# Performance work log

Hardware: AMD Instinct MI355X
Metric: run time of the kernel (lower is better)

Reference implementation:

```python
import jax, jax.numpy as jnp
import numpy as np

N = 50000       # nodes
E = 1600000     # edges (before self-loops)
NFEAT = 256
NHID = 8        # hidden units per head
HEADS = 8
NCLASS = 16
L1 = 0.5        # damping lambda layer 1
L2 = 0.5        # damping lambda layer 2
SLOPE = 0.2     # LeakyReLU negative slope (PyG GATConv default)


def setup_inputs() -> dict:
    ks = jax.random.split(jax.random.key(0), 16)
    g = lambda k, shape, fan: jax.random.normal(k, shape, jnp.float32) * (1.0 / np.sqrt(fan))
    return {
        "x": jax.random.normal(ks[0], (N, NFEAT), jnp.float32),
        "edge_index": jax.random.randint(ks[1], (2, E), 0, N, jnp.int64),
        # conv1: GATConv(nfeat -> nhid, heads=HEADS, concat=True)
        "W1": g(ks[2], (NFEAT, HEADS * NHID), NFEAT),
        "a1_src": g(ks[3], (HEADS, NHID), NHID),
        "a1_dst": g(ks[4], (HEADS, NHID), NHID),
        "b1": jnp.zeros((HEADS * NHID,), jnp.float32),
        # conv2: GATConv(nhid*heads -> nclass, heads=1, concat=False)
        "W2": g(ks[5], (HEADS * NHID, NCLASS), HEADS * NHID),
        "a2_src": g(ks[6], (1, NCLASS), NCLASS),
        "a2_dst": g(ks[7], (1, NCLASS), NCLASS),
        "b2": jnp.zeros((NCLASS,), jnp.float32),
        # side-branch linear layers
        "fc1_W": g(ks[8], (NFEAT, NHID), NFEAT),
        "fc1_b": jnp.zeros((NHID,), jnp.float32),
        "fc2_W": g(ks[9], (HEADS * NHID, NCLASS), HEADS * NHID),
        "fc2_b": jnp.zeros((NCLASS,), jnp.float32),
    }


def gat_conv(x, W, a_src, a_dst, b, src, dst, heads, outc, concat):
    n = x.shape[0]
    h = (x @ W).reshape(n, heads, outc)                 # [N, H, C]
    alpha_s = jnp.sum(h * a_src, axis=-1)               # [N, H]
    alpha_d = jnp.sum(h * a_dst, axis=-1)               # [N, H]
    e = jax.nn.leaky_relu(alpha_s[src] + alpha_d[dst], SLOPE)  # [Etot, H]
    # segment softmax over incoming edges of each destination node
    m = jax.ops.segment_max(e, dst, num_segments=n)
    m = jax.lax.stop_gradient(m)                        # max-shift is grad-neutral
    ex = jnp.exp(e - m[dst])
    denom = jax.ops.segment_sum(ex, dst, num_segments=n)
    alpha = ex / denom[dst]                             # [Etot, H]
    out = jax.ops.segment_sum(h[src] * alpha[:, :, None], dst, num_segments=n)
    if concat:
        out = out.reshape(n, heads * outc)
    else:
        out = out.mean(axis=1)
    return out + b


def reference(x, edge_index, W1, a1_src, a1_dst, b1, W2, a2_src, a2_dst, b2,
              fc1_W, fc1_b, fc2_W, fc2_b):
    loop = jnp.arange(N, dtype=edge_index.dtype)
    src = jnp.concatenate([edge_index[0], loop])
    dst = jnp.concatenate([edge_index[1], loop])
    # layer 1: GATConv + damped linear side branch
    out1 = gat_conv(x, W1, a1_src, a1_dst, b1, src, dst, HEADS, NHID, True)
    side1 = jnp.tile(x @ fc1_W + fc1_b, (1, HEADS))     # cat of heads copies
    h = jax.nn.elu(out1 - L1 * side1)                   # [N, H*C]
    # layer 2
    out2 = gat_conv(h, W2, a2_src, a2_dst, b2, src, dst, 1, NCLASS, False)
    side2 = h @ fc2_W + fc2_b
    return jax.nn.log_softmax(out2 - L2 * side2, axis=1)
```

## Files before the change

kernel.cpp:

```cpp
#include <hip/hip_runtime.h>
#include <hip/hip_bf16.h>
#include <cstddef>

constexpr int N      = 50000;
constexpr int E      = 1600000;
constexpr int NFEAT  = 256;
constexpr float SLOPE = 0.2f;
constexpr float L1d  = 0.5f;
constexpr float L2d  = 0.5f;

constexpr int BSHIFT = 7;
constexpr int NBUK   = (N + 127) >> BSHIFT;
constexpr int EPB    = 4096;
constexpr int NBLK   = (E + EPB - 1) / EPB;
constexpr int CAP    = 5120;

constexpr size_t al64(size_t x) { return (x + 63) & ~size_t(63); }
constexpr size_t W_OFFS  = 0;
constexpr size_t W_CSR   = W_OFFS  + al64(N + 1);
constexpr size_t W_STAGE = W_CSR   + (size_t)E;
constexpr size_t W_BHIST = W_STAGE + (size_t)E;
constexpr size_t W_TOT   = W_BHIST + al64((size_t)NBLK * NBUK);
constexpr size_t W_BBASE = W_TOT   + al64(NBUK);
constexpr size_t W_H1B   = W_BBASE + al64(NBUK + 1);
constexpr size_t W_S1B   = W_H1B   + (size_t)N * 32;
constexpr size_t W_D1    = W_S1B   + (size_t)N * 4;
constexpr size_t W_SIDE1 = W_D1    + (size_t)N * 8;
constexpr size_t W_HF    = W_SIDE1 + (size_t)N * 8;
constexpr size_t W_H2B   = W_HF    + (size_t)N * 64;
constexpr size_t W_SIDE2 = W_H2B   + (size_t)N * 8;
constexpr size_t W_S2B   = W_SIDE2 + (size_t)N * 16;
constexpr size_t W_D2    = W_S2B   + al64(N / 2);

typedef short bf16x8 __attribute__((ext_vector_type(8)));
typedef float f32x4  __attribute__((ext_vector_type(4)));

__device__ inline short f2bf(float f) {
    unsigned u = __builtin_bit_cast(unsigned, f);
    u += 0x7FFF + ((u >> 16) & 1);
    return (short)(u >> 16);
}

__device__ inline float bfu2f(unsigned short u) {
    return __builtin_bit_cast(float, (unsigned)u << 16);
}


__global__ __launch_bounds__(256) void p1_hist_kernel(const int* __restrict__ ei,
                                                      int* __restrict__ bhist) {
    __shared__ int hist[NBUK];
    int tid = threadIdx.x;
    for (int j = tid; j < NBUK; j += 256) hist[j] = 0;
    __syncthreads();
    int base = blockIdx.x * EPB;
    int end = base + EPB; if (end > E) end = E;
    for (int i = base + tid; i < end; i += 256) {
        int d = ei[E + i];
        atomicAdd(&hist[d >> BSHIFT], 1);
    }
    __syncthreads();
    for (int j = tid; j < NBUK; j += 256) bhist[(size_t)blockIdx.x * NBUK + j] = hist[j];
}

__global__ __launch_bounds__(512) void s1_scan_kernel(int* __restrict__ bhist,
                                                      int* __restrict__ tot) {
    __shared__ int sd[512];
    int tid = threadIdx.x;
    int b = blockIdx.x;
    int v = (tid < NBLK) ? bhist[(size_t)tid * NBUK + b] : 0;
    sd[tid] = v;
    __syncthreads();
    for (int off = 1; off < 512; off <<= 1) {
        int t = (tid >= off) ? sd[tid - off] : 0;
        __syncthreads();
        sd[tid] += t;
        __syncthreads();
    }
    if (tid < NBLK) bhist[(size_t)tid * NBUK + b] = sd[tid] - v;
    if (tid == 511) tot[b] = sd[511];
}

__global__ __launch_bounds__(512) void s2_scan_kernel(const int* __restrict__ tot,
                                                      int* __restrict__ bbase,
                                                      int* __restrict__ offs) {
    __shared__ int sd[512];
    int tid = threadIdx.x;
    int v = (tid < NBUK) ? tot[tid] : 0;
    sd[tid] = v;
    __syncthreads();
    for (int off = 1; off < 512; off <<= 1) {
        int t = (tid >= off) ? sd[tid - off] : 0;
        __syncthreads();
        sd[tid] += t;
        __syncthreads();
    }
    if (tid < NBUK) bbase[tid] = sd[tid] - v;
    if (tid == 0) { bbase[NBUK] = E; offs[N] = E; }
}

__global__ __launch_bounds__(256) void p2_stage_kernel(const int* __restrict__ ei,
                                                       const int* __restrict__ bhist,
                                                       const int* __restrict__ bbase,
                                                       unsigned int* __restrict__ stage) {
    __shared__ int cur[NBUK];
    int tid = threadIdx.x;
    for (int j = tid; j < NBUK; j += 256)
        cur[j] = bbase[j] + bhist[(size_t)blockIdx.x * NBUK + j];
    __syncthreads();
    int base = blockIdx.x * EPB;
    int end = base + EPB; if (end > E) end = E;
    for (int i = base + tid; i < end; i += 256) {
        int s = ei[i];
        int d = ei[E + i];
        int b = d >> BSHIFT;
        int pos = atomicAdd(&cur[b], 1);
        stage[pos] = ((unsigned int)(d & 127) << 24) | (unsigned int)s;
    }
}

__global__ __launch_bounds__(256) void p3_fine_kernel(const unsigned int* __restrict__ stage,
                                                      const int* __restrict__ bbase,
                                                      int* __restrict__ offs,
                                                      int* __restrict__ csr) {
    __shared__ unsigned int sstage[CAP];
    __shared__ int hist[128];
    __shared__ int scn[128];
    __shared__ int cur[128];
    int tid = threadIdx.x;
    int b = blockIdx.x;
    int ebase = bbase[b], eend = bbase[b + 1];
    int cnt = eend - ebase;
    if (tid < 128) hist[tid] = 0;
    __syncthreads();
    for (int i = tid; i < cnt; i += 256) {
        unsigned int p = stage[ebase + i];
        if (i < CAP) sstage[i] = p;
        atomicAdd(&hist[p >> 24], 1);
    }
    __syncthreads();
    if (tid < 128) scn[tid] = hist[tid];
    __syncthreads();
    for (int off = 1; off < 128; off <<= 1) {
        int t = (tid < 128 && tid >= off) ? scn[tid - off] : 0;
        __syncthreads();
        if (tid < 128) scn[tid] += t;
        __syncthreads();
    }
    if (tid < 128) {
        int excl = scn[tid] - hist[tid];
        cur[tid] = excl;
        int v = (b << BSHIFT) + tid;
        if (v < N) offs[v] = ebase + excl;
    }
    __syncthreads();
    for (int i = tid; i < cnt; i += 256) {
        unsigned int p = (i < CAP) ? sstage[i] : stage[ebase + i];
        int dloc = (int)(p >> 24);
        int s = (int)(p & 0xFFFFFFu);
        int r = atomicAdd(&cur[dloc], 1);
        csr[ebase + r] = s;
    }
}

__global__ __launch_bounds__(256) void gemm1_kernel(const float* __restrict__ x,
                                                    const float* __restrict__ W1,
                                                    const float* __restrict__ fc1W,
                                                    const float* __restrict__ fc1b,
                                                    short* __restrict__ h1b,
                                                    float* __restrict__ side1) {
    __shared__ bf16x8 wfrag[2560];
    int tid = threadIdx.x;

    for (int s = tid; s < 2560; s += 256) {
        int l = s & 63;
        int t = s >> 6;
        int nt = t % 5, kt = t / 5;
        int col = nt * 16 + (l & 15);
        int kbase = kt * 32 + (l >> 4) * 8;
        bf16x8 v;
#pragma unroll
        for (int j = 0; j < 8; ++j) {
            float f = 0.f;
            if (col < 64)      f = W1[(size_t)(kbase + j) * 64 + col];
            else if (col < 72) f = fc1W[(size_t)(kbase + j) * 8 + (col - 64)];
            v[j] = f2bf(f);
        }
        wfrag[s] = v;
    }
    __syncthreads();

    int w = tid >> 6;
    int l = tid & 63;
    int row0 = blockIdx.x * 64;
    int arow = row0 + w * 16 + (l & 15);
    if (arow >= N) arow = N - 1;
    const float* ap = x + (size_t)arow * NFEAT + ((l >> 4) * 8);

    f32x4 acc[5];
#pragma unroll
    for (int nt = 0; nt < 5; ++nt) acc[nt] = (f32x4){0.f, 0.f, 0.f, 0.f};

#pragma unroll
    for (int kt = 0; kt < 8; ++kt) {
        float4 alo = *reinterpret_cast<const float4*>(ap + kt * 32);
        float4 ahi = *reinterpret_cast<const float4*>(ap + kt * 32 + 4);
        bf16x8 af;
        af[0] = f2bf(alo.x); af[1] = f2bf(alo.y); af[2] = f2bf(alo.z); af[3] = f2bf(alo.w);
        af[4] = f2bf(ahi.x); af[5] = f2bf(ahi.y); af[6] = f2bf(ahi.z); af[7] = f2bf(ahi.w);
#pragma unroll
        for (int nt = 0; nt < 5; ++nt) {
            acc[nt] = __builtin_amdgcn_mfma_f32_16x16x32_bf16(
                af, wfrag[(kt * 5 + nt) * 64 + l], acc[nt], 0, 0, 0);
        }
    }

    int cbase = l & 15;
    int rbase = row0 + w * 16 + (l >> 4) * 4;
#pragma unroll
    for (int nt = 0; nt < 4; ++nt) {
#pragma unroll
        for (int r = 0; r < 4; ++r) {
            int row = rbase + r;
            if (row < N) h1b[(size_t)row * 64 + nt * 16 + cbase] = f2bf(acc[nt][r]);
        }
    }
    if (cbase < 8) {
        float bb = fc1b[cbase];
#pragma unroll
        for (int r = 0; r < 4; ++r) {
            int row = rbase + r;
            if (row < N) side1[(size_t)row * 8 + cbase] = acc[4][r] + bb;
        }
    }
}

__global__ __launch_bounds__(256) void alpha1_kernel(const __hip_bfloat16* __restrict__ h1b,
                                                     const float* __restrict__ a1s,
                                                     const float* __restrict__ a1d,
                                                     __hip_bfloat16* __restrict__ s1b,
                                                     float* __restrict__ d1) {
    int wave = threadIdx.x >> 6;
    int lane = threadIdx.x & 63;
    int v = blockIdx.x * 4 + wave;
    if (v >= N) return;
    float hv = __bfloat162float(h1b[(size_t)v * 64 + lane]);
    float sa = hv * a1s[lane];
    float sd = hv * a1d[lane];
#pragma unroll
    for (int off = 1; off < 8; off <<= 1) {
        sa += __shfl_xor(sa, off, 64);
        sd += __shfl_xor(sd, off, 64);
    }
    if ((lane & 7) == 0) {
        s1b[v * 8 + (lane >> 3)] = __float2bfloat16(sa);
        d1[v * 8 + (lane >> 3)] = sd;
    }
}

__global__ __launch_bounds__(256) void agg1_kernel(const int* __restrict__ offs,
                                                   const int* __restrict__ csr,
                                                   const unsigned short* __restrict__ h1u,
                                                   const unsigned short* __restrict__ s1u,
                                                   const float* __restrict__ d1,
                                                   const float* __restrict__ side1,
                                                   const float* __restrict__ b1,
                                                   float* __restrict__ hf) {
    int wave = threadIdx.x >> 6;
    int lane = threadIdx.x & 63;
    int v = blockIdx.x * 4 + wave;
    if (v >= N) return;
    int j  = lane >> 3;
    int hh = lane & 7;
    int hc = lane >> 3;

    float dv_att = d1[v * 8 + hh];
    float dv_ch  = __shfl(dv_att, hc, 64);

    float e0 = bfu2f(s1u[v * 8 + hc]) + dv_ch;
    e0 = fmaxf(e0, SLOPE * e0);
    float ex0 = __expf(e0);
    float acc = ex0 * bfu2f(h1u[(size_t)v * 64 + lane]);
    float den0 = ex0;
    float den_att = 0.f;

    int beg = offs[v], end = offs[v + 1];
    int deg = end - beg;
    int ng = (deg + 7) >> 3;

    auto csrg = [&](int g) {
        int idx = beg + g * 8 + j;
        idx = idx < end - 1 ? idx : end - 1;
        idx = idx > 0 ? idx : 0;
        return csr[idx];
    };

    unsigned short hA[8], hB[8];
    int sA = 0, sB = 0;
    float svA = 0.f, svB = 0.f;

    if (ng > 0) {
        sA = csrg(0);
        svA = bfu2f(s1u[sA * 8 + hh]);
#pragma unroll
        for (int jj = 0; jj < 8; ++jj) {
            int sj = __builtin_amdgcn_readlane(sA, jj * 8);
            const unsigned short* p = h1u + ((size_t)sj << 6);
            hA[jj] = p[lane];
        }
        sB = csrg(1);
    }

    int g = 0;
    for (; g + 1 < ng; g += 2) {
        svB = bfu2f(s1u[sB * 8 + hh]);
#pragma unroll
        for (int jj = 0; jj < 8; ++jj) {
            int sj = __builtin_amdgcn_readlane(sB, jj * 8);
            const unsigned short* p = h1u + ((size_t)sj << 6);
            hB[jj] = p[lane];
        }
        int sC = csrg(g + 2);
        {
            float a = svA + dv_att;
            a = fmaxf(a, SLOPE * a);
            float xv = __expf(a);
            xv = (beg + g * 8 + j < end) ? xv : 0.f;
            den_att += xv;
#pragma unroll
            for (int jj = 0; jj < 8; ++jj) {
                float xj = __shfl(xv, jj * 8 + hc, 64);
                acc += xj * bfu2f(hA[jj]);
            }
        }
        sA = sC;
        svA = bfu2f(s1u[sA * 8 + hh]);
#pragma unroll
        for (int jj = 0; jj < 8; ++jj) {
            int sj = __builtin_amdgcn_readlane(sA, jj * 8);
            const unsigned short* p = h1u + ((size_t)sj << 6);
            hA[jj] = p[lane];
        }
        int sD = csrg(g + 3);
        {
            float a = svB + dv_att;
            a = fmaxf(a, SLOPE * a);
            float xv = __expf(a);
            xv = (beg + (g + 1) * 8 + j < end) ? xv : 0.f;
            den_att += xv;
#pragma unroll
            for (int jj = 0; jj < 8; ++jj) {
                float xj = __shfl(xv, jj * 8 + hc, 64);
                acc += xj * bfu2f(hB[jj]);
            }
        }
        sB = sD;
    }
    if (g < ng) {
        float a = svA + dv_att;
        a = fmaxf(a, SLOPE * a);
        float xv = __expf(a);
        xv = (beg + g * 8 + j < end) ? xv : 0.f;
        den_att += xv;
#pragma unroll
        for (int jj = 0; jj < 8; ++jj) {
            float xj = __shfl(xv, jj * 8 + hc, 64);
            acc += xj * bfu2f(hA[jj]);
        }
    }

    den_att += __shfl_xor(den_att, 8, 64);
    den_att += __shfl_xor(den_att, 16, 64);
    den_att += __shfl_xor(den_att, 32, 64);
    float den = den0 + __shfl(den_att, hc, 64);

    float o = acc / den + b1[lane];
    float z = o - L1d * side1[v * 8 + (lane & 7)];
    hf[(size_t)v * 64 + lane] = z > 0.f ? z : (__expf(z) - 1.f);
}

__global__ __launch_bounds__(256) void gemm2_kernel(const float* __restrict__ hf,
                                                    const float* __restrict__ W2,
                                                    const float* __restrict__ fc2W,
                                                    const float* __restrict__ fc2b,
                                                    __hip_bfloat16* __restrict__ h2b,
                                                    float* __restrict__ side2) {
    __shared__ float xs[128][65];
    __shared__ float ws[64][33];
    int tid = threadIdx.x;
    int ty = tid >> 3;
    int tx = tid & 7;
    int row0 = blockIdx.x * 128;

    float acc[4][4];
#pragma unroll
    for (int i = 0; i < 4; ++i)
#pragma unroll
        for (int j = 0; j < 4; ++j) acc[i][j] = 0.f;

    int lr = tid >> 4;
    int lj = tid & 15;
#pragma unroll
    for (int it = 0; it < 8; ++it) {
        int r = lr + it * 16;
        int grow = row0 + r;
        if (grow >= N) grow = N - 1;
        float4 vv = *reinterpret_cast<const float4*>(&hf[(size_t)grow * 64 + lj * 4]);
        xs[r][lj * 4 + 0] = vv.x;
        xs[r][lj * 4 + 1] = vv.y;
        xs[r][lj * 4 + 2] = vv.z;
        xs[r][lj * 4 + 3] = vv.w;
    }
    for (int idx = tid; idx < 64 * 32; idx += 256) {
        int k = idx >> 5;
        int c = idx & 31;
        float v = (c < 16) ? W2[(size_t)k * 16 + c] : fc2W[(size_t)k * 16 + (c - 16)];
        ws[k][c] = v;
    }
    __syncthreads();
#pragma unroll 4
    for (int k = 0; k < 64; ++k) {
        float xv[4], wv[4];
#pragma unroll
        for (int i = 0; i < 4; ++i) xv[i] = xs[ty * 4 + i][k];
#pragma unroll
        for (int j = 0; j < 4; ++j) wv[j] = ws[k][tx * 4 + j];
#pragma unroll
        for (int i = 0; i < 4; ++i)
#pragma unroll
            for (int j = 0; j < 4; ++j) acc[i][j] += xv[i] * wv[j];
    }

#pragma unroll
    for (int i = 0; i < 4; ++i) {
        int row = row0 + ty * 4 + i;
        if (row >= N) continue;
#pragma unroll
        for (int j = 0; j < 4; ++j) {
            int c = tx * 4 + j;
            if (c < 16) h2b[(size_t)row * 16 + c] = __float2bfloat16(acc[i][j]);
            else        side2[(size_t)row * 16 + (c - 16)] = acc[i][j] + fc2b[c - 16];
        }
    }
}

__global__ __launch_bounds__(256) void alpha2_kernel(const __hip_bfloat16* __restrict__ h2b,
                                                     const float* __restrict__ a2s,
                                                     const float* __restrict__ a2d,
                                                     __hip_bfloat16* __restrict__ s2b,
                                                     float* __restrict__ d2) {
    int wave = threadIdx.x >> 6;
    int lane = threadIdx.x & 63;
    int vbase = (blockIdx.x * 4 + wave) * 4;
    int r = lane >> 4;
    int c = lane & 15;
    int v = vbase + r;
    float hv = (v < N) ? __bfloat162float(h2b[(size_t)v * 16 + c]) : 0.f;
    float sa = hv * a2s[c];
    float sd = hv * a2d[c];
#pragma unroll
    for (int off = 1; off < 16; off <<= 1) {
        sa += __shfl_xor(sa, off, 64);
        sd += __shfl_xor(sd, off, 64);
    }
    if (v < N && c == 0) {
        s2b[v] = __float2bfloat16(sa);
        d2[v] = sd;
    }
}

__global__ __launch_bounds__(256) void agg2_kernel(const int* __restrict__ offs,
                                                   const int* __restrict__ csr,
                                                   const unsigned short* __restrict__ h2u,
                                                   const unsigned short* __restrict__ s2u,
                                                   const float* __restrict__ d2,
                                                   const float* __restrict__ side2,
                                                   const float* __restrict__ b2,
                                                   float* __restrict__ out) {
    int wave = threadIdx.x >> 6;
    int lane = threadIdx.x & 63;
    int v = blockIdx.x * 4 + wave;
    if (v >= N) return;
    int c = lane & 15;
    int slot = lane >> 4;
    float dv = d2[v];

    float acc = 0.f, den = 0.f;
    if (slot == 0) {
        float e = bfu2f(s2u[v]) + dv;
        e = fmaxf(e, SLOPE * e);
        float ex = __expf(e);
        acc = ex * bfu2f(h2u[(size_t)v * 16 + c]);
        den = ex;
    }
    int beg = offs[v], end = offs[v + 1];
    int deg = end - beg;
    int ng = (deg + 3) >> 2;

    auto csrg = [&](int g) {
        int idx = beg + g * 4 + slot;
        idx = idx < end - 1 ? idx : end - 1;
        idx = idx > 0 ? idx : 0;
        return csr[idx];
    };

    int sA = 0, sB = 0;
    float svA = 0.f, svB = 0.f, hvA = 0.f, hvB = 0.f;
    if (ng > 0) {
        sA = csrg(0);
        svA = bfu2f(s2u[sA]);
        hvA = bfu2f(h2u[(size_t)sA * 16 + c]);
        sB = csrg(1);
    }
    int g = 0;
    for (; g + 1 < ng; g += 2) {
        svB = bfu2f(s2u[sB]);
        hvB = bfu2f(h2u[(size_t)sB * 16 + c]);
        int sC = csrg(g + 2);
        {
            float a = svA + dv;
            a = fmaxf(a, SLOPE * a);
            float x = __expf(a);
            x = (beg + g * 4 + slot < end) ? x : 0.f;
            acc += x * hvA;
            den += x;
        }
        sA = sC;
        svA = bfu2f(s2u[sA]);
        hvA = bfu2f(h2u[(size_t)sA * 16 + c]);
        int sD = csrg(g + 3);
        {
            float a = svB + dv;
            a = fmaxf(a, SLOPE * a);
            float x = __expf(a);
            x = (beg + (g + 1) * 4 + slot < end) ? x : 0.f;
            acc += x * hvB;
            den += x;
        }
        sB = sD;
    }
    if (g < ng) {
        float a = svA + dv;
        a = fmaxf(a, SLOPE * a);
        float x = __expf(a);
        x = (beg + g * 4 + slot < end) ? x : 0.f;
        acc += x * hvA;
        den += x;
    }

    acc += __shfl_xor(acc, 16, 64);
    acc += __shfl_xor(acc, 32, 64);
    den += __shfl_xor(den, 16, 64);
    den += __shfl_xor(den, 32, 64);

    float o = acc / den + b2[c];
    float z = o - L2d * side2[(size_t)v * 16 + c];

    float m = z;
#pragma unroll
    for (int off = 1; off < 16; off <<= 1) m = fmaxf(m, __shfl_xor(m, off, 64));
    float ex = __expf(z - m);
    float s = ex;
#pragma unroll
    for (int off = 1; off < 16; off <<= 1) s += __shfl_xor(s, off, 64);
    float lsm = z - m - __logf(s);
    if (slot == 0) out[(size_t)v * 16 + c] = lsm;
}

extern "C" void kernel_launch(void* const* d_in, const int* in_sizes, int n_in,
                              void* d_out, int out_size, void* d_ws, size_t ws_size,
                              hipStream_t stream) {
    const float* x    = (const float*)d_in[0];
    const int*   ei   = (const int*)d_in[1];
    const float* W1   = (const float*)d_in[2];
    const float* a1s  = (const float*)d_in[3];
    const float* a1d  = (const float*)d_in[4];
    const float* b1   = (const float*)d_in[5];
    const float* W2   = (const float*)d_in[6];
    const float* a2s  = (const float*)d_in[7];
    const float* a2d  = (const float*)d_in[8];
    const float* b2   = (const float*)d_in[9];
    const float* fc1W = (const float*)d_in[10];
    const float* fc1b = (const float*)d_in[11];
    const float* fc2W = (const float*)d_in[12];
    const float* fc2b = (const float*)d_in[13];
    float* out = (float*)d_out;

    int*   wsi = (int*)d_ws;
    float* wsf = (float*)d_ws;
    int*   offs   = wsi + W_OFFS;
    int*   csr    = wsi + W_CSR;
    unsigned int* stage = (unsigned int*)(wsi + W_STAGE);
    int*   bhist  = wsi + W_BHIST;
    int*   tot    = wsi + W_TOT;
    int*   bbase  = wsi + W_BBASE;
    __hip_bfloat16* h1b = (__hip_bfloat16*)(wsf + W_H1B);
    __hip_bfloat16* s1b = (__hip_bfloat16*)(wsf + W_S1B);
    float* d1     = wsf + W_D1;
    float* side1  = wsf + W_SIDE1;
    float* hf     = wsf + W_HF;
    __hip_bfloat16* h2b = (__hip_bfloat16*)(wsf + W_H2B);
    float* side2  = wsf + W_SIDE2;
    __hip_bfloat16* s2b = (__hip_bfloat16*)(wsf + W_S2B);
    float* d2     = wsf + W_D2;

    p1_hist_kernel<<<NBLK, 256, 0, stream>>>(ei, bhist);
    s1_scan_kernel<<<NBUK, 512, 0, stream>>>(bhist, tot);
    s2_scan_kernel<<<1, 512, 0, stream>>>(tot, bbase, offs);
    p2_stage_kernel<<<NBLK, 256, 0, stream>>>(ei, bhist, bbase, stage);
    p3_fine_kernel<<<NBUK, 256, 0, stream>>>(stage, bbase, offs, csr);

    gemm1_kernel<<<(N + 63) / 64, 256, 0, stream>>>(x, W1, fc1W, fc1b,
                                                    (short*)h1b, side1);
    alpha1_kernel<<<(N + 3) / 4, 256, 0, stream>>>(h1b, a1s, a1d, s1b, d1);
    agg1_kernel<<<(N + 3) / 4, 256, 0, stream>>>(offs, csr,
                                                 (const unsigned short*)h1b,
                                                 (const unsigned short*)s1b,
                                                 d1, side1, b1, hf);

    gemm2_kernel<<<(N + 127) / 128, 256, 0, stream>>>(hf, W2, fc2W, fc2b, h2b, side2);
    alpha2_kernel<<<(N + 15) / 16, 256, 0, stream>>>(h2b, a2s, a2d, s2b, d2);
    agg2_kernel<<<(N + 3) / 4, 256, 0, stream>>>(offs, csr,
                                                 (const unsigned short*)h2b,
                                                 (const unsigned short*)s2b,
                                                 d2, side2, b2, out);
}
```

Measured before the change: 156.7 us.

## Restructure layer-1 aggregation to per-lane redundant attention with scalar CSR reads

Rewrites the layer-1 aggregation so every lane computes the attention weight for its own head, rather than one lane per edge/head pair followed by shuffle broadcasts. Neighbor indices come from uniform CSR loads via readfirstlane, in groups of four, with a two-stage software pipeline and a scalar tail loop. This removes the per-edge shuffles and the final cross-lane denominator reduction. In exchange it runs eight times as many exp evaluations and issues a separate s1 gather per lane.

```diff
diff --git a/kernel.cpp b/kernel.cpp
--- a/kernel.cpp
+++ b/kernel.cpp
@@ -265,117 +265,92 @@
                                                    const float* __restrict__ side1,
                                                    const float* __restrict__ b1,
                                                    float* __restrict__ hf) {
-    int wave = threadIdx.x >> 6;
     int lane = threadIdx.x & 63;
-    int v = blockIdx.x * 4 + wave;
+    int v = blockIdx.x * 4 + (threadIdx.x >> 6);
     if (v >= N) return;
-    int j  = lane >> 3;
-    int hh = lane & 7;
-    int hc = lane >> 3;
-
-    float dv_att = d1[v * 8 + hh];
-    float dv_ch  = __shfl(dv_att, hc, 64);
-
-    float e0 = bfu2f(s1u[v * 8 + hc]) + dv_ch;
+    int hh = lane >> 3;
+
+    float dv = d1[v * 8 + hh];
+    float e0 = bfu2f(s1u[v * 8 + hh]) + dv;
     e0 = fmaxf(e0, SLOPE * e0);
     float ex0 = __expf(e0);
-    float acc = ex0 * bfu2f(h1u[(size_t)v * 64 + lane]);
-    float den0 = ex0;
-    float den_att = 0.f;
+    float acc = ex0 * bfu2f(h1u[((size_t)v << 6) + lane]);
+    float den = ex0;
 
     int beg = offs[v], end = offs[v + 1];
     int deg = end - beg;
-    int ng = (deg + 7) >> 3;
-
-    auto csrg = [&](int g) {
-        int idx = beg + g * 8 + j;
-        idx = idx < end - 1 ? idx : end - 1;
-        idx = idx > 0 ? idx : 0;
-        return csr[idx];
-    };
-
-    unsigned short hA[8], hB[8];
-    int sA = 0, sB = 0;
-    float svA = 0.f, svB = 0.f;
-
-    if (ng > 0) {
-        sA = csrg(0);
-        svA = bfu2f(s1u[sA * 8 + hh]);
-#pragma unroll
-        for (int jj = 0; jj < 8; ++jj) {
-            int sj = __builtin_amdgcn_readlane(sA, jj * 8);
-            const unsigned short* p = h1u + ((size_t)sj << 6);
-            hA[jj] = p[lane];
-        }
-        sB = csrg(1);
-    }
-
+    int ngf = deg >> 2;
+    const int* cb = csr + beg;
+
+    int sA0, sA1, sA2, sA3, sB0, sB1, sB2, sB3;
+    unsigned short svA0, svA1, svA2, svA3, hvA0, hvA1, hvA2, hvA3;
+    unsigned short svB0, svB1, svB2, svB3, hvB0, hvB1, hvB2, hvB3;
+
+#define RFL4(s0, s1_, s2_, s3_, p)                                           \
+    do {                                                                     \
+        s0  = __builtin_amdgcn_readfirstlane((p)[0]);                        \
+        s1_ = __builtin_amdgcn_readfirstlane((p)[1]);                        \
+        s2_ = __builtin_amdgcn_readfirstlane((p)[2]);                        \
+        s3_ = __builtin_amdgcn_readfirstlane((p)[3]);                        \
+    } while (0)
+
+#define LOADS4(sv0, sv1, sv2, sv3, hv0, hv1, hv2, hv3, s0, s1_, s2_, s3_)    \
+    do {                                                                     \
+        sv0 = s1u[(size_t)(s0) * 8 + hh];                                    \
+        sv1 = s1u[(size_t)(s1_) * 8 + hh];                                   \
+        sv2 = s1u[(size_t)(s2_) * 8 + hh];                                   \
+        sv3 = s1u[(size_t)(s3_) * 8 + hh];                                   \
+        hv0 = h1u[((size_t)(s0) << 6) + lane];                               \
+        hv1 = h1u[((size_t)(s1_) << 6) + lane];                              \
+        hv2 = h1u[((size_t)(s2_) << 6) + lane];                              \
+        hv3 = h1u[((size_t)(s3_) << 6) + lane];                              \
+    } while (0)
+
+#define COMP4(sv0, sv1, sv2, sv3, hv0, hv1, hv2, hv3)                        \
+    do {                                                                     \
+        float a0 = bfu2f(sv0) + dv; a0 = fmaxf(a0, SLOPE * a0);              \
+        float a1 = bfu2f(sv1) + dv; a1 = fmaxf(a1, SLOPE * a1);              \
+        float a2 = bfu2f(sv2) + dv; a2 = fmaxf(a2, SLOPE * a2);              \
+        float a3 = bfu2f(sv3) + dv; a3 = fmaxf(a3, SLOPE * a3);              \
+        float x0 = __expf(a0), x1 = __expf(a1), x2 = __expf(a2), x3 = __expf(a3); \
+        acc += x0 * bfu2f(hv0); den += x0;                                   \
+        acc += x1 * bfu2f(hv1); den += x1;                                   \
+        acc += x2 * bfu2f(hv2); den += x2;                                   \
+        acc += x3 * bfu2f(hv3); den += x3;                                   \
+    } while (0)
+
+    if (ngf > 0) {
+        RFL4(sA0, sA1, sA2, sA3, cb);
+        LOADS4(svA0, svA1, svA2, svA3, hvA0, hvA1, hvA2, hvA3, sA0, sA1, sA2, sA3);
+        if (ngf > 1) RFL4(sB0, sB1, sB2, sB3, cb + 4);
+    }
     int g = 0;
-    for (; g + 1 < ng; g += 2) {
-        svB = bfu2f(s1u[sB * 8 + hh]);
-#pragma unroll
-        for (int jj = 0; jj < 8; ++jj) {
-            int sj = __builtin_amdgcn_readlane(sB, jj * 8);
-            const unsigned short* p = h1u + ((size_t)sj << 6);
-            hB[jj] = p[lane];
-        }
-        int sC = csrg(g + 2);
-        {
-            float a = svA + dv_att;
-            a = fmaxf(a, SLOPE * a);
-            float xv = __expf(a);
-            xv = (beg + g * 8 + j < end) ? xv : 0.f;
-            den_att += xv;
-#pragma unroll
-            for (int jj = 0; jj < 8; ++jj) {
-                float xj = __shfl(xv, jj * 8 + hc, 64);
-                acc += xj * bfu2f(hA[jj]);
-            }
-        }
-        sA = sC;
-        svA = bfu2f(s1u[sA * 8 + hh]);
-#pragma unroll
-        for (int jj = 0; jj < 8; ++jj) {
-            int sj = __builtin_amdgcn_readlane(sA, jj * 8);
-            const unsigned short* p = h1u + ((size_t)sj << 6);
-            hA[jj] = p[lane];
-        }
-        int sD = csrg(g + 3);
-        {
-            float a = svB + dv_att;
-            a = fmaxf(a, SLOPE * a);
-            float xv = __expf(a);
-            xv = (beg + (g + 1) * 8 + j < end) ? xv : 0.f;
-            den_att += xv;
-#pragma unroll
-            for (int jj = 0; jj < 8; ++jj) {
-                float xj = __shfl(xv, jj * 8 + hc, 64);
-                acc += xj * bfu2f(hB[jj]);
-            }
-        }
-        sB = sD;
-    }
-    if (g < ng) {
-        float a = svA + dv_att;
+    for (; g + 1 < ngf; g += 2) {
+        LOADS4(svB0, svB1, svB2, svB3, hvB0, hvB1, hvB2, hvB3, sB0, sB1, sB2, sB3);
+        if (g + 2 < ngf) RFL4(sA0, sA1, sA2, sA3, cb + (g + 2) * 4);
+        COMP4(svA0, svA1, svA2, svA3, hvA0, hvA1, hvA2, hvA3);
+        if (g + 2 < ngf)
+            LOADS4(svA0, svA1, svA2, svA3, hvA0, hvA1, hvA2, hvA3, sA0, sA1, sA2, sA3);
+        if (g + 3 < ngf) RFL4(sB0, sB1, sB2, sB3, cb + (g + 3) * 4);
+        COMP4(svB0, svB1, svB2, svB3, hvB0, hvB1, hvB2, hvB3);
+    }
+    if (g < ngf) COMP4(svA0, svA1, svA2, svA3, hvA0, hvA1, hvA2, hvA3);
+
+    for (int t = ngf * 4; t < deg; ++t) {
+        int s = __builtin_amdgcn_readfirstlane(cb[t]);
+        float a = bfu2f(s1u[(size_t)s * 8 + hh]) + dv;
         a = fmaxf(a, SLOPE * a);
-        float xv = __expf(a);
-        xv = (beg + g * 8 + j < end) ? xv : 0.f;
-        den_att += xv;
-#pragma unroll
-        for (int jj = 0; jj < 8; ++jj) {
-            float xj = __shfl(xv, jj * 8 + hc, 64);
-            acc += xj * bfu2f(hA[jj]);
-        }
-    }
-
-    den_att += __shfl_xor(den_att, 8, 64);
-    den_att += __shfl_xor(den_att, 16, 64);
-    den_att += __shfl_xor(den_att, 32, 64);
-    float den = den0 + __shfl(den_att, hc, 64);
+        float xx = __expf(a);
+        acc += xx * bfu2f(h1u[((size_t)s << 6) + lane]);
+        den += xx;
+    }
+#undef RFL4
+#undef LOADS4
+#undef COMP4
 
     float o = acc / den + b1[lane];
     float z = o - L1d * side1[v * 8 + (lane & 7)];
-    hf[(size_t)v * 64 + lane] = z > 0.f ? z : (__expf(z) - 1.f);
+    hf[((size_t)v << 6) + lane] = z > 0.f ? z : (__expf(z) - 1.f);
 }
 
 __global__ __launch_bounds__(256) void gemm2_kernel(const float* __restrict__ hf,
```

After: 177.7 us. 1.13x slower.

## Store layer-1 output in bf16 and compute layer-2 GEMM with MFMA

Applied to the files above, without the earlier changes.

agg1 now writes the ELU output as bf16 instead of fp32, which halves the intermediate traffic. gemm2 is rewritten to use bf16 MFMA 16x16x32 with the weight fragments preloaded into LDS, replacing the fp32 LDS-tiled scalar GEMM. agg2's edge loop is split into full groups with no per-edge mask or clamping plus one masked remainder pass. The load and compute sequences in agg1 are moved into macros. The cost is extra bf16 rounding of the hidden activations and of W2.

```diff
diff --git a/kernel.cpp b/kernel.cpp
--- a/kernel.cpp
+++ b/kernel.cpp
@@ -26,8 +26,8 @@
 constexpr size_t W_S1B   = W_H1B   + (size_t)N * 32;
 constexpr size_t W_D1    = W_S1B   + (size_t)N * 4;
 constexpr size_t W_SIDE1 = W_D1    + (size_t)N * 8;
-constexpr size_t W_HF    = W_SIDE1 + (size_t)N * 8;
-constexpr size_t W_H2B   = W_HF    + (size_t)N * 64;
+constexpr size_t W_HFB   = W_SIDE1 + (size_t)N * 8;
+constexpr size_t W_H2B   = W_HFB   + (size_t)N * 32;
 constexpr size_t W_SIDE2 = W_H2B   + (size_t)N * 8;
 constexpr size_t W_S2B   = W_SIDE2 + (size_t)N * 16;
 constexpr size_t W_D2    = W_S2B   + al64(N / 2);
@@ -264,7 +264,7 @@
                                                    const float* __restrict__ d1,
                                                    const float* __restrict__ side1,
                                                    const float* __restrict__ b1,
-                                                   float* __restrict__ hf) {
+                                                   short* __restrict__ hfb) {
     int wave = threadIdx.x >> 6;
     int lane = threadIdx.x & 63;
     int v = blockIdx.x * 4 + wave;
@@ -298,75 +298,63 @@
     int sA = 0, sB = 0;
     float svA = 0.f, svB = 0.f;
 
+#define LOADH(s8, h)                                                        \
+    do {                                                                     \
+        int sj0 = __builtin_amdgcn_readlane(s8, 0);                          \
+        int sj1 = __builtin_amdgcn_readlane(s8, 8);                          \
+        int sj2 = __builtin_amdgcn_readlane(s8, 16);                         \
+        int sj3 = __builtin_amdgcn_readlane(s8, 24);                         \
+        int sj4 = __builtin_amdgcn_readlane(s8, 32);                         \
+        int sj5 = __builtin_amdgcn_readlane(s8, 40);                         \
+        int sj6 = __builtin_amdgcn_readlane(s8, 48);                         \
+        int sj7 = __builtin_amdgcn_readlane(s8, 56);                         \
+        h[0] = h1u[((size_t)sj0 << 6) + lane];                               \
+        h[1] = h1u[((size_t)sj1 << 6) + lane];                               \
+        h[2] = h1u[((size_t)sj2 << 6) + lane];                               \
+        h[3] = h1u[((size_t)sj3 << 6) + lane];                               \
+        h[4] = h1u[((size_t)sj4 << 6) + lane];                               \
+        h[5] = h1u[((size_t)sj5 << 6) + lane];                               \
+        h[6] = h1u[((size_t)sj6 << 6) + lane];                               \
+        h[7] = h1u[((size_t)sj7 << 6) + lane];                               \
+    } while (0)
+
+#define COMP(sv, h, gidx)                                                    \
+    do {                                                                     \
+        float a = (sv) + dv_att;                                             \
+        a = fmaxf(a, SLOPE * a);                                             \
+        float xv = __expf(a);                                                \
+        xv = (beg + (gidx) * 8 + j < end) ? xv : 0.f;                        \
+        den_att += xv;                                                       \
+        _Pragma("unroll")                                                    \
+        for (int jj = 0; jj < 8; ++jj) {                                     \
+            float xj = __shfl(xv, jj * 8 + hc, 64);                          \
+            acc += xj * bfu2f(h[jj]);                                        \
+        }                                                                    \
+    } while (0)
+
     if (ng > 0) {
         sA = csrg(0);
         svA = bfu2f(s1u[sA * 8 + hh]);
-#pragma unroll
-        for (int jj = 0; jj < 8; ++jj) {
-            int sj = __builtin_amdgcn_readlane(sA, jj * 8);
-            const unsigned short* p = h1u + ((size_t)sj << 6);
-            hA[jj] = p[lane];
-        }
+        LOADH(sA, hA);
         sB = csrg(1);
     }
 
     int g = 0;
     for (; g + 1 < ng; g += 2) {
         svB = bfu2f(s1u[sB * 8 + hh]);
-#pragma unroll
-        for (int jj = 0; jj < 8; ++jj) {
-            int sj = __builtin_amdgcn_readlane(sB, jj * 8);
-            const unsigned short* p = h1u + ((size_t)sj << 6);
-            hB[jj] = p[lane];
-        }
+        LOADH(sB, hB);
         int sC = csrg(g + 2);
-        {
-            float a = svA + dv_att;
-            a = fmaxf(a, SLOPE * a);
-            float xv = __expf(a);
-            xv = (beg + g * 8 + j < end) ? xv : 0.f;
-            den_att += xv;
-#pragma unroll
-            for (int jj = 0; jj < 8; ++jj) {
-                float xj = __shfl(xv, jj * 8 + hc, 64);
-                acc += xj * bfu2f(hA[jj]);
-            }
-        }
+        COMP(svA, hA, g);
         sA = sC;
         svA = bfu2f(s1u[sA * 8 + hh]);
-#pragma unroll
-        for (int jj = 0; jj < 8; ++jj) {
-            int sj = __builtin_amdgcn_readlane(sA, jj * 8);
-            const unsigned short* p = h1u + ((size_t)sj << 6);
-            hA[jj] = p[lane];
-        }
+        LOADH(sA, hA);
         int sD = csrg(g + 3);
-        {
-            float a = svB + dv_att;
-            a = fmaxf(a, SLOPE * a);
-            float xv = __expf(a);
-            xv = (beg + (g + 1) * 8 + j < end) ? xv : 0.f;
-            den_att += xv;
-#pragma unroll
-            for (int jj = 0; jj < 8; ++jj) {
-                float xj = __shfl(xv, jj * 8 + hc, 64);
-                acc += xj * bfu2f(hB[jj]);
-            }
-        }
+        COMP(svB, hB, g + 1);
         sB = sD;
     }
-    if (g < ng) {
-        float a = svA + dv_att;
-        a = fmaxf(a, SLOPE * a);
-        float xv = __expf(a);
-        xv = (beg + g * 8 + j < end) ? xv : 0.f;
-        den_att += xv;
-#pragma unroll
-        for (int jj = 0; jj < 8; ++jj) {
-            float xj = __shfl(xv, jj * 8 + hc, 64);
-            acc += xj * bfu2f(hA[jj]);
-        }
-    }
+    if (g < ng) COMP(svA, hA, g);
+#undef LOADH
+#undef COMP
 
     den_att += __shfl_xor(den_att, 8, 64);
     den_att += __shfl_xor(den_att, 16, 64);
@@ -375,70 +363,66 @@
 
     float o = acc / den + b1[lane];
     float z = o - L1d * side1[v * 8 + (lane & 7)];
-    hf[(size_t)v * 64 + lane] = z > 0.f ? z : (__expf(z) - 1.f);
-}
-
-__global__ __launch_bounds__(256) void gemm2_kernel(const float* __restrict__ hf,
+    hfb[(size_t)v * 64 + lane] = f2bf(z > 0.f ? z : (__expf(z) - 1.f));
+}
+
+__global__ __launch_bounds__(256) void gemm2_kernel(const unsigned short* __restrict__ hfb,
                                                     const float* __restrict__ W2,
                                                     const float* __restrict__ fc2W,
                                                     const float* __restrict__ fc2b,
-                                                    __hip_bfloat16* __restrict__ h2b,
+                                                    short* __restrict__ h2b,
                                                     float* __restrict__ side2) {
-    __shared__ float xs[128][65];
-    __shared__ float ws[64][33];
+    __shared__ bf16x8 wfrag[256];
     int tid = threadIdx.x;
-    int ty = tid >> 3;
-    int tx = tid & 7;
-    int row0 = blockIdx.x * 128;
-
-    float acc[4][4];
-#pragma unroll
-    for (int i = 0; i < 4; ++i)
-#pragma unroll
-        for (int j = 0; j < 4; ++j) acc[i][j] = 0.f;
-
-    int lr = tid >> 4;
-    int lj = tid & 15;
-#pragma unroll
-    for (int it = 0; it < 8; ++it) {
-        int r = lr + it * 16;
-        int grow = row0 + r;
-        if (grow >= N) grow = N - 1;
-        float4 vv = *reinterpret_cast<const float4*>(&hf[(size_t)grow * 64 + lj * 4]);
-        xs[r][lj * 4 + 0] = vv.x;
-        xs[r][lj * 4 + 1] = vv.y;
-        xs[r][lj * 4 + 2] = vv.z;
-        xs[r][lj * 4 + 3] = vv.w;
-    }
-    for (int idx = tid; idx < 64 * 32; idx += 256) {
-        int k = idx >> 5;
-        int c = idx & 31;
-        float v = (c < 16) ? W2[(size_t)k * 16 + c] : fc2W[(size_t)k * 16 + (c - 16)];
-        ws[k][c] = v;
-    }
-    __syncthreads();
-#pragma unroll 4
-    for (int k = 0; k < 64; ++k) {
-        float xv[4], wv[4];
-#pragma unroll
-        for (int i = 0; i < 4; ++i) xv[i] = xs[ty * 4 + i][k];
-#pragma unroll
-        for (int j = 0; j < 4; ++j) wv[j] = ws[k][tx * 4 + j];
-#pragma unroll
-        for (int i = 0; i < 4; ++i)
-#pragma unroll
-            for (int j = 0; j < 4; ++j) acc[i][j] += xv[i] * wv[j];
-    }
-
-#pragma unroll
-    for (int i = 0; i < 4; ++i) {
-        int row = row0 + ty * 4 + i;
-        if (row >= N) continue;
-#pragma unroll
-        for (int j = 0; j < 4; ++j) {
-            int c = tx * 4 + j;
-            if (c < 16) h2b[(size_t)row * 16 + c] = __float2bfloat16(acc[i][j]);
-            else        side2[(size_t)row * 16 + (c - 16)] = acc[i][j] + fc2b[c - 16];
+
+    if (tid < 256) {
+        int s = tid;
+        int l = s & 63;
+        int t = s >> 6;
+        int nt = t & 1, kt = t >> 1;
+        int col = nt * 16 + (l & 15);
+        int kbase = kt * 32 + (l >> 4) * 8;
+        bf16x8 v;
+#pragma unroll
+        for (int j = 0; j < 8; ++j) {
+            float f = (col < 16) ? W2[(size_t)(kbase + j) * 16 + col]
+                                 : fc2W[(size_t)(kbase + j) * 16 + (col - 16)];
+            v[j] = f2bf(f);
+        }
+        wfrag[s] = v;
+    }
+    __syncthreads();
+
+    int w = tid >> 6;
+    int l = tid & 63;
+    int row0 = blockIdx.x * 64;
+    int arow = row0 + w * 16 + (l & 15);
+    if (arow >= N) arow = N - 1;
+    const unsigned short* ap = hfb + (size_t)arow * 64 + ((l >> 4) * 8);
+
+    f32x4 acc[2];
+    acc[0] = (f32x4){0.f, 0.f, 0.f, 0.f};
+    acc[1] = (f32x4){0.f, 0.f, 0.f, 0.f};
+
+#pragma unroll
+    for (int kt = 0; kt < 2; ++kt) {
+        bf16x8 af = *reinterpret_cast<const bf16x8*>(ap + kt * 32);
+#pragma unroll
+        for (int nt = 0; nt < 2; ++nt) {
+            acc[nt] = __builtin_amdgcn_mfma_f32_16x16x32_bf16(
+                af, wfrag[(kt * 2 + nt) * 64 + l], acc[nt], 0, 0, 0);
+        }
+    }
+
+    int cbase = l & 15;
+    int rbase = row0 + w * 16 + (l >> 4) * 4;
+    float bb = fc2b[cbase];
+#pragma unroll
+    for (int r = 0; r < 4; ++r) {
+        int row = rbase + r;
+        if (row < N) {
+            h2b[(size_t)row * 16 + cbase] = f2bf(acc[0][r]);
+            side2[(size_t)row * 16 + cbase] = acc[1][r] + bb;
         }
     }
 }
@@ -494,56 +478,61 @@
     }
     int beg = offs[v], end = offs[v + 1];
     int deg = end - beg;
-    int ng = (deg + 3) >> 2;
-
-    auto csrg = [&](int g) {
-        int idx = beg + g * 4 + slot;
-        idx = idx < end - 1 ? idx : end - 1;
-        idx = idx > 0 ? idx : 0;
-        return csr[idx];
-    };
+    int ngf = deg >> 2;
+    int rem = deg & 3;
+    const int* cb = csr + beg;
 
     int sA = 0, sB = 0;
     float svA = 0.f, svB = 0.f, hvA = 0.f, hvB = 0.f;
-    if (ng > 0) {
-        sA = csrg(0);
+    if (ngf > 0) {
+        sA = cb[slot];
         svA = bfu2f(s2u[sA]);
         hvA = bfu2f(h2u[(size_t)sA * 16 + c]);
-        sB = csrg(1);
+        if (ngf > 1) sB = cb[4 + slot];
     }
     int g = 0;
-    for (; g + 1 < ng; g += 2) {
+    for (; g + 1 < ngf; g += 2) {
         svB = bfu2f(s2u[sB]);
         hvB = bfu2f(h2u[(size_t)sB * 16 + c]);
-        int sC = csrg(g + 2);
+        int sC = (g + 2 < ngf) ? cb[(g + 2) * 4 + slot] : 0;
         {
             float a = svA + dv;
             a = fmaxf(a, SLOPE * a);
             float x = __expf(a);
-            x = (beg + g * 4 + slot < end) ? x : 0.f;
             acc += x * hvA;
             den += x;
         }
         sA = sC;
-        svA = bfu2f(s2u[sA]);
-        hvA = bfu2f(h2u[(size_t)sA * 16 + c]);
-        int sD = csrg(g + 3);
+        if (g + 2 < ngf) {
+            svA = bfu2f(s2u[sA]);
+            hvA = bfu2f(h2u[(size_t)sA * 16 + c]);
+        }
+        int sD = (g + 3 < ngf) ? cb[(g + 3) * 4 + slot] : 0;
         {
             float a = svB + dv;
             a = fmaxf(a, SLOPE * a);
             float x = __expf(a);
-            x = (beg + (g + 1) * 4 + slot < end) ? x : 0.f;
             acc += x * hvB;
             den += x;
         }
         sB = sD;
     }
-    if (g < ng) {
+    if (g < ngf) {
         float a = svA + dv;
         a = fmaxf(a, SLOPE * a);
         float x = __expf(a);
-        x = (beg + g * 4 + slot < end) ? x : 0.f;
         acc += x * hvA;
+        den += x;
+    }
+    if (rem) {
+        int idx = beg + ngf * 4 + slot;
+        idx = idx < end ? idx : end - 1;
+        int s = csr[idx];
+        float a = bfu2f(s2u[s]) + dv;
+        a = fmaxf(a, SLOPE * a);
+        float x = __expf(a);
+        x = (slot < rem) ? x : 0.f;
+        acc += x * bfu2f(h2u[(size_t)s * 16 + c]);
         den += x;
     }
 
@@ -597,7 +586,7 @@
     __hip_bfloat16* s1b = (__hip_bfloat16*)(wsf + W_S1B);
     float* d1     = wsf + W_D1;
     float* side1  = wsf + W_SIDE1;
-    float* hf     = wsf + W_HF;
+    short* hfb    = (short*)(wsf + W_HFB);
     __hip_bfloat16* h2b = (__hip_bfloat16*)(wsf + W_H2B);
     float* side2  = wsf + W_SIDE2;
     __hip_bfloat16* s2b = (__hip_bfloat16*)(wsf + W_S2B);
@@ -615,9 +604,11 @@
     agg1_kernel<<<(N + 3) / 4, 256, 0, stream>>>(offs, csr,
                                                  (const unsigned short*)h1b,
                                                  (const unsigned short*)s1b,
-                                                 d1, side1, b1, hf);
-
-    gemm2_kernel<<<(N + 127) / 128, 256, 0, stream>>>(hf, W2, fc2W, fc2b, h2b, side2);
+                                                 d1, side1, b1, hfb);
+
+    gemm2_kernel<<<(N + 63) / 64, 256, 0, stream>>>((const unsigned short*)hfb,
+                                                    W2, fc2W, fc2b,
+                                                    (short*)h2b, side2);
     alpha2_kernel<<<(N + 15) / 16, 256, 0, stream>>>(h2b, a2s, a2d, s2b, d2);
     agg2_kernel<<<(N + 3) / 4, 256, 0, stream>>>(offs, csr,
                                                  (const unsigned short*)h2b,
```

New measurement: 155.4 us. About the same (-0.8%).
